# Kernel optimization log

Measured on AMD Instinct MI355X. Metric: run time of the kernel, lower is better.

Reference implementation:

```python
import jax, jax.numpy as jnp
import numpy as np

H = 1024      # hidden_size
I = 4096      # intermediate_size
E = 8         # num_experts
TOP_K = 2
LB_COEF = 0.01


def setup_inputs() -> dict:
    key = jax.random.key(0)
    ks = jax.random.split(key, 8)
    s_h = 1.0 / np.sqrt(H)
    s_i = 1.0 / np.sqrt(I)
    return {
        "x": jax.random.normal(ks[0], (2, 2048, H), dtype=jnp.float32),
        "Wr": jax.random.normal(ks[1], (H, E), dtype=jnp.float32) * s_h,
        "br": jnp.zeros((E,), dtype=jnp.float32),
        "W1": jax.random.normal(ks[2], (E, H, I), dtype=jnp.float32) * s_h,
        "b1": jnp.zeros((E, I), dtype=jnp.float32),
        "W2": jax.random.normal(ks[3], (E, I, H), dtype=jnp.float32) * s_i,
        "b2": jnp.zeros((E, H), dtype=jnp.float32),
    }


def _moe_forward(x, Wr, br, W1, b1, W2, b2):
    B, S, Hd = x.shape
    x_flat = x.reshape(-1, Hd)                      # [T, H]
    T = x_flat.shape[0]

    # ---- Router: softmax probs, top-k, renormalize ----
    logits = x_flat @ Wr + br                       # [T, E]
    probs = jax.nn.softmax(logits, axis=-1)         # [T, E]
    topk_w, topk_idx = jax.lax.top_k(probs, TOP_K)  # [T, K]
    topk_w = topk_w / jnp.sum(topk_w, axis=-1, keepdims=True)

    # ---- Load-balance aux loss (switch-style) ----
    onehot = jax.nn.one_hot(topk_idx, E, dtype=x.dtype)   # [T, K, E]
    frac_tokens = onehot.mean(axis=(0, 1))                 # [E]
    frac_probs = probs.mean(axis=0)                        # [E]
    aux_loss = E * jnp.sum(frac_tokens * frac_probs) * LB_COEF

    # combine_weights[t, e] = routing weight of expert e for token t (0 if unselected)
    combine = jnp.sum(topk_w[..., None] * onehot, axis=1)  # [T, E]

    # ---- Experts: dense per-expert FFN, weighted combine ----
    out = jnp.zeros_like(x_flat)
    for e in range(E):
        h = jax.nn.gelu(x_flat @ W1[e] + b1[e])            # [T, I]
        y = h @ W2[e] + b2[e]                              # [T, H]
        out = out + y * combine[:, e:e + 1]
    return out.reshape(B, S, Hd), aux_loss


def reference(x, Wr, br, W1, b1, W2, b2):
    return _moe_forward(x, Wr, br, W1, b1, W2, b2)
```

## Files before the change

kernel.cpp:

```cpp
#include <hip/hip_runtime.h>
#include <hip/hip_bf16.h>

#define HD 1024
#define ID 4096
#define NE 8
#define NT 4096
#define NSLOT (NT*2)

typedef __attribute__((ext_vector_type(4))) float f32x4;
typedef __attribute__((ext_vector_type(8))) short bf16x8;
typedef __attribute__((ext_vector_type(4))) unsigned int u32x4;
typedef __attribute__((ext_vector_type(2))) unsigned int u32x2;
typedef unsigned short u16;

__device__ __forceinline__ u16 f2b(float f) {
  __hip_bfloat16 h = __float2bfloat16(f);
  return __builtin_bit_cast(unsigned short, h);
}
__device__ __forceinline__ unsigned int pack2(float a, float b) {
  return (unsigned int)f2b(a) | ((unsigned int)f2b(b) << 16);
}
__device__ __forceinline__ void gload16(const void* g, void* l) {
  __builtin_amdgcn_global_load_lds(
      (const __attribute__((address_space(1))) unsigned int*)g,
      (__attribute__((address_space(3))) unsigned int*)l, 16, 0, 0);
}
__device__ __forceinline__ float gelu_tanh(float v) {
  float c = v + 0.044715f * v * v * v;
  return 0.5f * v * (1.0f + tanhf(0.7978845608028654f * c));
}

__global__ void k_convert_x(const float* __restrict__ x, u16* __restrict__ xb) {
  int i = blockIdx.x * 256 + threadIdx.x;
  const f32x4* x4 = (const f32x4*)x;
  f32x4 a = x4[2 * i], b = x4[2 * i + 1];
  u32x4 r;
  r[0] = pack2(a[0], a[1]); r[1] = pack2(a[2], a[3]);
  r[2] = pack2(b[0], b[1]); r[3] = pack2(b[2], b[3]);
  ((u32x4*)xb)[i] = r;
}

__global__ __launch_bounds__(256) void k_transpose_bf16(
    const float* __restrict__ src, u16* __restrict__ dst, int R, int C) {
  __shared__ float tile[64][65];
  int e = blockIdx.z;
  int c0 = blockIdx.x * 64;
  int r0 = blockIdx.y * 64;
  int t = threadIdx.x;
  const float* s = src + (size_t)e * R * C;
#pragma unroll
  for (int i = 0; i < 16; ++i) {
    int r = i * 4 + (t >> 6);
    tile[r][t & 63] = s[(size_t)(r0 + r) * C + c0 + (t & 63)];
  }
  __syncthreads();
  u16* d = dst + (size_t)e * R * C;
#pragma unroll
  for (int i = 0; i < 4; ++i) {
    int c = i * 16 + (t >> 4);
    int rb = (t & 15) * 4;
    u32x2 p;
    p[0] = pack2(tile[rb + 0][c], tile[rb + 1][c]);
    p[1] = pack2(tile[rb + 2][c], tile[rb + 3][c]);
    *(u32x2*)&d[(size_t)(c0 + c) * R + r0 + rb] = p;
  }
}

__global__ __launch_bounds__(256) void k_router(
    const float* __restrict__ x, const float* __restrict__ Wr,
    const float* __restrict__ br, int* __restrict__ cnt,
    int* __restrict__ slotE, int* __restrict__ slotLoc,
    float* __restrict__ slotW, float* __restrict__ probsAll) {
  __shared__ float wrt[NE * HD];
  int t = threadIdx.x;
  for (int i = t; i < NE * HD; i += 256) wrt[(i & 7) * HD + (i >> 3)] = Wr[i];
  __syncthreads();
  int wave = t >> 6, lane = t & 63;
  int token = blockIdx.x * 4 + wave;
  const float* xr = x + (size_t)token * HD;
  float acc[NE] = {0, 0, 0, 0, 0, 0, 0, 0};
#pragma unroll 4
  for (int j = 0; j < 16; ++j) {
    int h = j * 64 + lane;
    float xv = xr[h];
#pragma unroll
    for (int e = 0; e < NE; ++e) acc[e] += xv * wrt[e * HD + h];
  }
#pragma unroll
  for (int d = 1; d < 64; d <<= 1) {
#pragma unroll
    for (int e = 0; e < NE; ++e) acc[e] += __shfl_xor(acc[e], d, 64);
  }
  if (lane == 0) {
    float lg[NE], p[NE];
    float m = -1e30f;
#pragma unroll
    for (int e = 0; e < NE; ++e) { lg[e] = acc[e] + br[e]; m = fmaxf(m, lg[e]); }
    float s = 0.f;
#pragma unroll
    for (int e = 0; e < NE; ++e) { p[e] = expf(lg[e] - m); s += p[e]; }
    float inv = 1.0f / s;
    int i1 = 0, i2 = -1;
    float v1 = -1.f, v2 = -1.f;
#pragma unroll
    for (int e = 0; e < NE; ++e) {
      p[e] *= inv;
      probsAll[token * NE + e] = p[e];
      if (p[e] > v1) { v2 = v1; i2 = i1; v1 = p[e]; i1 = e; }
      else if (p[e] > v2) { v2 = p[e]; i2 = e; }
    }
    float wsum = v1 + v2;
    int l1 = atomicAdd(&cnt[i1], 1);
    int l2 = atomicAdd(&cnt[i2], 1);
    slotE[token * 2] = i1;     slotLoc[token * 2] = l1;     slotW[token * 2] = v1 / wsum;
    slotE[token * 2 + 1] = i2; slotLoc[token * 2 + 1] = l2; slotW[token * 2 + 1] = v2 / wsum;
  }
}

__global__ __launch_bounds__(256) void k_finalize(
    const float* __restrict__ probsAll, const int* __restrict__ cnt,
    int* __restrict__ off, float* __restrict__ out_aux) {
  __shared__ float red[256];
  int t = threadIdx.x;
  float loc[NE] = {0, 0, 0, 0, 0, 0, 0, 0};
  for (int i = t; i < NT; i += 256) {
#pragma unroll
    for (int e = 0; e < NE; ++e) loc[e] += probsAll[i * NE + e];
  }
  __shared__ float psum[NE];
  for (int e = 0; e < NE; ++e) {
    red[t] = loc[e];
    __syncthreads();
    for (int s = 128; s > 0; s >>= 1) {
      if (t < s) red[t] += red[t + s];
      __syncthreads();
    }
    if (t == 0) psum[e] = red[0];
    __syncthreads();
  }
  if (t == 0) {
    int o = 0;
    float a = 0.f;
    for (int e = 0; e < NE; ++e) {
      off[e] = o;
      o += cnt[e];
      a += ((float)cnt[e] / (float)NSLOT) * (psum[e] / (float)NT);
    }
    off[NE] = o;
    out_aux[0] = (float)NE * a * 0.01f;
  }
}

__global__ void k_scatter(const int* __restrict__ slotE, const int* __restrict__ slotLoc,
                          const float* __restrict__ slotW, const int* __restrict__ off,
                          int* __restrict__ rowTok, float* __restrict__ rowW) {
  int i = blockIdx.x * 256 + threadIdx.x;
  int pos = off[slotE[i]] + slotLoc[i];
  if (pos < 0) pos = 0;
  if (pos >= NSLOT) pos = NSLOT - 1;
  rowTok[pos] = i >> 1;
  rowW[pos] = slotW[i];
}

__global__ __launch_bounds__(256, 2) void k_gemm1(
    const u16* __restrict__ xb, const u16* __restrict__ w1t,
    const float* __restrict__ b1, u16* __restrict__ hbuf,
    const int* __restrict__ cnt, const int* __restrict__ off,
    const int* __restrict__ rowTok) {
  const int NWG = NE * 32 * 32;
  int bid = blockIdx.x;
  int wg = (bid & 7) * (NWG / 8) + (bid >> 3);
  int e = wg >> 10;
  int rem = wg & 1023;
  int m0 = (rem >> 5) * 128;
  int n0 = (rem & 31) * 128;
  int ce = cnt[e];
  if (m0 >= ce) return;
  int oe = off[e];
  __shared__ u16 As[2][128 * 32];
  __shared__ u16 Bs[2][128 * 32];
  __shared__ int rtok[128];
  int t = threadIdx.x;
  if (t < 128) {
    int r = m0 + t;
    if (r >= ce) r = ce - 1;
    int tok = rowTok[oe + r];
    rtok[t] = (tok < 0) ? 0 : (tok >= NT ? NT - 1 : tok);
  }
  __syncthreads();
  int c0 = t, c1 = t + 256;
  const u16* srcA0 = xb + (size_t)rtok[c0 >> 2] * HD + (c0 & 3) * 8;
  const u16* srcA1 = xb + (size_t)rtok[c1 >> 2] * HD + (c1 & 3) * 8;
  const u16* bb = w1t + (size_t)e * ID * HD + (size_t)n0 * HD;
  const u16* srcB0 = bb + (size_t)(c0 >> 2) * HD + (c0 & 3) * 8;
  const u16* srcB1 = bb + (size_t)(c1 >> 2) * HD + (c1 & 3) * 8;
  int wave = t >> 6, lane = t & 63;
  int wr = wave >> 1, wc = wave & 1;
  int aoff = (wr * 64 + (lane & 15)) * 32 + (lane >> 4) * 8;
  int boff = (wc * 64 + (lane & 15)) * 32 + (lane >> 4) * 8;
  f32x4 acc[4][4] = {};
  const int NK = HD / 32;
  gload16(srcA0, &As[0][c0 * 8]);
  gload16(srcA1, &As[0][c1 * 8]);
  gload16(srcB0, &Bs[0][c0 * 8]);
  gload16(srcB1, &Bs[0][c1 * 8]);
  srcA0 += 32; srcA1 += 32; srcB0 += 32; srcB1 += 32;
  __syncthreads();
  int cur = 0;
  for (int kt = 0;;) {
    if (kt + 1 < NK) {
      int nb = cur ^ 1;
      gload16(srcA0, &As[nb][c0 * 8]);
      gload16(srcA1, &As[nb][c1 * 8]);
      gload16(srcB0, &Bs[nb][c0 * 8]);
      gload16(srcB1, &Bs[nb][c1 * 8]);
      srcA0 += 32; srcA1 += 32; srcB0 += 32; srcB1 += 32;
    }
    const u16* ap = &As[cur][aoff];
    const u16* bp = &Bs[cur][boff];
    bf16x8 af[4], bfr[4];
#pragma unroll
    for (int m = 0; m < 4; ++m) af[m] = *(const bf16x8*)(ap + m * 16 * 32);
#pragma unroll
    for (int n = 0; n < 4; ++n) bfr[n] = *(const bf16x8*)(bp + n * 16 * 32);
#pragma unroll
    for (int m = 0; m < 4; ++m)
#pragma unroll
      for (int n = 0; n < 4; ++n)
        acc[m][n] = __builtin_amdgcn_mfma_f32_16x16x32_bf16(af[m], bfr[n], acc[m][n], 0, 0, 0);
    if (++kt == NK) break;
    __syncthreads();
    cur ^= 1;
  }
  const float* b1e = b1 + (size_t)e * ID + n0;
#pragma unroll
  for (int n = 0; n < 4; ++n) {
    int col = wc * 64 + n * 16 + (lane & 15);
    float bias = b1e[col];
#pragma unroll
    for (int m = 0; m < 4; ++m) {
      int rbase = wr * 64 + m * 16 + (lane >> 4) * 4;
#pragma unroll
      for (int r = 0; r < 4; ++r) {
        int grow = m0 + rbase + r;
        if (grow < ce) {
          float v = acc[m][n][r] + bias;
          hbuf[(size_t)(oe + grow) * ID + n0 + col] = f2b(gelu_tanh(v));
        }
      }
    }
  }
}

__global__ __launch_bounds__(256, 2) void k_gemm2(
    const u16* __restrict__ hbuf, const u16* __restrict__ w2t,
    const float* __restrict__ b2, float* __restrict__ out,
    const int* __restrict__ cnt, const int* __restrict__ off,
    const int* __restrict__ rowTok, const float* __restrict__ rowW) {
  const int NWG = NE * 32 * 2 * 8;
  int bid = blockIdx.x;
  int wg = (bid & 7) * (NWG / 8) + (bid >> 3);
  int e = wg >> 9;
  int rem = wg & 511;
  int m0 = (rem >> 4) * 128;
  int ks = (rem >> 3) & 1;
  int n0 = (rem & 7) * 128;
  int ce = cnt[e];
  if (m0 >= ce) return;
  int oe = off[e];
  int k0 = ks * (ID / 2);
  __shared__ u16 As[2][128 * 32];
  __shared__ u16 Bs[2][128 * 32];
  __shared__ int rtok[128];
  __shared__ float rw[128];
  int t = threadIdx.x;
  if (t < 128) {
    int r = m0 + t;
    int rc = (r < ce) ? r : ce - 1;
    int tok = rowTok[oe + rc];
    rtok[t] = (tok < 0) ? 0 : (tok >= NT ? NT - 1 : tok);
    rw[t] = (r < ce) ? rowW[oe + r] : 0.0f;
  }
  __syncthreads();
  int c0 = t, c1 = t + 256;
  int rA0 = m0 + (c0 >> 2); if (rA0 >= ce) rA0 = ce - 1;
  int rA1 = m0 + (c1 >> 2); if (rA1 >= ce) rA1 = ce - 1;
  const u16* srcA0 = hbuf + (size_t)(oe + rA0) * ID + k0 + (c0 & 3) * 8;
  const u16* srcA1 = hbuf + (size_t)(oe + rA1) * ID + k0 + (c1 & 3) * 8;
  const u16* bb = w2t + (size_t)e * HD * ID + (size_t)n0 * ID + k0;
  const u16* srcB0 = bb + (size_t)(c0 >> 2) * ID + (c0 & 3) * 8;
  const u16* srcB1 = bb + (size_t)(c1 >> 2) * ID + (c1 & 3) * 8;
  int wave = t >> 6, lane = t & 63;
  int wr = wave >> 1, wc = wave & 1;
  int aoff = (wr * 64 + (lane & 15)) * 32 + (lane >> 4) * 8;
  int boff = (wc * 64 + (lane & 15)) * 32 + (lane >> 4) * 8;
  f32x4 acc[4][4] = {};
  const int NK = (ID / 2) / 32;
  gload16(srcA0, &As[0][c0 * 8]);
  gload16(srcA1, &As[0][c1 * 8]);
  gload16(srcB0, &Bs[0][c0 * 8]);
  gload16(srcB1, &Bs[0][c1 * 8]);
  srcA0 += 32; srcA1 += 32; srcB0 += 32; srcB1 += 32;
  __syncthreads();
  int cur = 0;
  for (int kt = 0;;) {
    if (kt + 1 < NK) {
      int nb = cur ^ 1;
      gload16(srcA0, &As[nb][c0 * 8]);
      gload16(srcA1, &As[nb][c1 * 8]);
      gload16(srcB0, &Bs[nb][c0 * 8]);
      gload16(srcB1, &Bs[nb][c1 * 8]);
      srcA0 += 32; srcA1 += 32; srcB0 += 32; srcB1 += 32;
    }
    const u16* ap = &As[cur][aoff];
    const u16* bp = &Bs[cur][boff];
    bf16x8 af[4], bfr[4];
#pragma unroll
    for (int m = 0; m < 4; ++m) af[m] = *(const bf16x8*)(ap + m * 16 * 32);
#pragma unroll
    for (int n = 0; n < 4; ++n) bfr[n] = *(const bf16x8*)(bp + n * 16 * 32);
#pragma unroll
    for (int m = 0; m < 4; ++m)
#pragma unroll
      for (int n = 0; n < 4; ++n)
        acc[m][n] = __builtin_amdgcn_mfma_f32_16x16x32_bf16(af[m], bfr[n], acc[m][n], 0, 0, 0);
    if (++kt == NK) break;
    __syncthreads();
    cur ^= 1;
  }
  const float* b2e = b2 + (size_t)e * HD + n0;
#pragma unroll
  for (int n = 0; n < 4; ++n) {
    int col = wc * 64 + n * 16 + (lane & 15);
    float bias = (ks == 0) ? b2e[col] : 0.0f;
#pragma unroll
    for (int m = 0; m < 4; ++m) {
      int rbase = wr * 64 + m * 16 + (lane >> 4) * 4;
#pragma unroll
      for (int r = 0; r < 4; ++r) {
        int grow = m0 + rbase + r;
        if (grow < ce) {
          float v = (acc[m][n][r] + bias) * rw[rbase + r];
          atomicAdd(&out[(size_t)rtok[rbase + r] * HD + n0 + col], v);
        }
      }
    }
  }
}

extern "C" void kernel_launch(void* const* d_in, const int* in_sizes, int n_in,
                              void* d_out, int out_size, void* d_ws, size_t ws_size,
                              hipStream_t stream) {
  const float* x  = (const float*)d_in[0];
  const float* Wr = (const float*)d_in[1];
  const float* br = (const float*)d_in[2];
  const float* W1 = (const float*)d_in[3];
  const float* b1 = (const float*)d_in[4];
  const float* W2 = (const float*)d_in[5];
  const float* b2 = (const float*)d_in[6];
  float* out = (float*)d_out;

  char* ws = (char*)d_ws;
  size_t o = 0;
  auto alloc = [&](size_t bytes) {
    void* p = ws + o;
    o = (o + bytes + 255) & ~(size_t)255;
    return p;
  };
  u16* xb    = (u16*)alloc((size_t)NT * HD * 2);
  u16* w1t   = (u16*)alloc((size_t)NE * ID * HD * 2);
  u16* w2t   = (u16*)alloc((size_t)NE * ID * HD * 2);
  u16* hbuf  = (u16*)alloc((size_t)NSLOT * ID * 2);
  int* cnt     = (int*)alloc(NE * 4);
  int* off     = (int*)alloc(16 * 4);
  int* slotE   = (int*)alloc(NSLOT * 4);
  int* slotLoc = (int*)alloc(NSLOT * 4);
  float* slotW = (float*)alloc(NSLOT * 4);
  int* rowTok  = (int*)alloc(NSLOT * 4);
  float* rowW  = (float*)alloc(NSLOT * 4);
  float* probsAll = (float*)alloc((size_t)NT * NE * 4);

  if (ws_size < o) return;

  hipMemsetAsync(cnt, 0, NE * 4, stream);
  hipMemsetAsync(out, 0, (size_t)out_size * 4, stream);
  k_convert_x<<<(NT * HD / 8) / 256, 256, 0, stream>>>(x, xb);
  k_transpose_bf16<<<dim3(ID / 64, HD / 64, NE), 256, 0, stream>>>(W1, w1t, HD, ID);
  k_transpose_bf16<<<dim3(HD / 64, ID / 64, NE), 256, 0, stream>>>(W2, w2t, ID, HD);
  k_router<<<NT / 4, 256, 0, stream>>>(x, Wr, br, cnt, slotE, slotLoc, slotW, probsAll);
  k_finalize<<<1, 256, 0, stream>>>(probsAll, cnt, off, out + (size_t)NT * HD);
  k_scatter<<<NSLOT / 256, 256, 0, stream>>>(slotE, slotLoc, slotW, off, rowTok, rowW);
  k_gemm1<<<NE * 32 * 32, 256, 0, stream>>>(xb, w1t, b1, hbuf, cnt, off, rowTok);
  k_gemm2<<<NE * 32 * 2 * 8, 256, 0, stream>>>(hbuf, w2t, b2, out, cnt, off, rowTok, rowW);
}
```

Baseline: 536.4 us.

## Swizzle LDS tiles, deepen GEMM prefetch pipeline, parallelize router prob reduction

Both expert GEMMs now apply an XOR swizzle to the LDS tile layout to avoid bank conflicts on the MFMA fragment reads. The double-buffered loop is restructured to issue two stages up front, with explicit vmcnt waits and raw barriers, so global-to-LDS loads overlap the MFMA work. Launch bounds move to 3 waves per SIMD for occupancy, which tightens register pressure. The single-block prob-sum finalize is split into a 32-block reduction with atomics plus a tiny finalize kernel, which adds one memset and one launch.

```diff
diff --git a/kernel.cpp b/kernel.cpp
--- a/kernel.cpp
+++ b/kernel.cpp
@@ -117,34 +117,31 @@
   }
 }
 
-__global__ __launch_bounds__(256) void k_finalize(
-    const float* __restrict__ probsAll, const int* __restrict__ cnt,
-    int* __restrict__ off, float* __restrict__ out_aux) {
+__global__ __launch_bounds__(256) void k_psum(const float* __restrict__ probsAll,
+                                              float* __restrict__ psumG) {
   __shared__ float red[256];
   int t = threadIdx.x;
-  float loc[NE] = {0, 0, 0, 0, 0, 0, 0, 0};
-  for (int i = t; i < NT; i += 256) {
-#pragma unroll
-    for (int e = 0; e < NE; ++e) loc[e] += probsAll[i * NE + e];
-  }
-  __shared__ float psum[NE];
-  for (int e = 0; e < NE; ++e) {
-    red[t] = loc[e];
+  int base = blockIdx.x * 128;
+  float s = 0.f;
+  for (int i = t >> 3; i < 128; i += 32) s += probsAll[(base + i) * NE + (t & 7)];
+  red[t] = s;
+  __syncthreads();
+  for (int st = 128; st >= 8; st >>= 1) {
+    if (t < st) red[t] += red[t + st];
     __syncthreads();
-    for (int s = 128; s > 0; s >>= 1) {
-      if (t < s) red[t] += red[t + s];
-      __syncthreads();
-    }
-    if (t == 0) psum[e] = red[0];
-    __syncthreads();
-  }
-  if (t == 0) {
+  }
+  if (t < 8) atomicAdd(&psumG[t], red[t]);
+}
+
+__global__ void k_finalize(const float* __restrict__ psumG, const int* __restrict__ cnt,
+                           int* __restrict__ off, float* __restrict__ out_aux) {
+  if (threadIdx.x == 0) {
     int o = 0;
     float a = 0.f;
     for (int e = 0; e < NE; ++e) {
       off[e] = o;
       o += cnt[e];
-      a += ((float)cnt[e] / (float)NSLOT) * (psum[e] / (float)NT);
+      a += ((float)cnt[e] / (float)NSLOT) * (psumG[e] / (float)NT);
     }
     off[NE] = o;
     out_aux[0] = (float)NE * a * 0.01f;
@@ -162,7 +159,15 @@
   rowW[pos] = slotW[i];
 }
 
-__global__ __launch_bounds__(256, 2) void k_gemm1(
+#define STG(bf) do { \
+    gload16(srcA0, &As[bf][c0 * 8]); \
+    gload16(srcA1, &As[bf][c1 * 8]); \
+    gload16(srcB0, &Bs[bf][c0 * 8]); \
+    gload16(srcB1, &Bs[bf][c1 * 8]); \
+    srcA0 += 32; srcA1 += 32; srcB0 += 32; srcB1 += 32; \
+  } while (0)
+
+__global__ __launch_bounds__(256, 3) void k_gemm1(
     const u16* __restrict__ xb, const u16* __restrict__ w1t,
     const float* __restrict__ b1, u16* __restrict__ hbuf,
     const int* __restrict__ cnt, const int* __restrict__ off,
@@ -189,35 +194,31 @@
   }
   __syncthreads();
   int c0 = t, c1 = t + 256;
-  const u16* srcA0 = xb + (size_t)rtok[c0 >> 2] * HD + (c0 & 3) * 8;
-  const u16* srcA1 = xb + (size_t)rtok[c1 >> 2] * HD + (c1 & 3) * 8;
+  int js0 = (c0 & 3) ^ ((c0 >> 3) & 3);
+  int js1 = (c1 & 3) ^ ((c1 >> 3) & 3);
+  const u16* srcA0 = xb + (size_t)rtok[c0 >> 2] * HD + js0 * 8;
+  const u16* srcA1 = xb + (size_t)rtok[c1 >> 2] * HD + js1 * 8;
   const u16* bb = w1t + (size_t)e * ID * HD + (size_t)n0 * HD;
-  const u16* srcB0 = bb + (size_t)(c0 >> 2) * HD + (c0 & 3) * 8;
-  const u16* srcB1 = bb + (size_t)(c1 >> 2) * HD + (c1 & 3) * 8;
+  const u16* srcB0 = bb + (size_t)(c0 >> 2) * HD + js0 * 8;
+  const u16* srcB1 = bb + (size_t)(c1 >> 2) * HD + js1 * 8;
   int wave = t >> 6, lane = t & 63;
   int wr = wave >> 1, wc = wave & 1;
-  int aoff = (wr * 64 + (lane & 15)) * 32 + (lane >> 4) * 8;
-  int boff = (wc * 64 + (lane & 15)) * 32 + (lane >> 4) * 8;
+  int arow = wr * 64 + (lane & 15);
+  int aoff = arow * 32 + ((lane >> 4) ^ ((arow >> 1) & 3)) * 8;
+  int brow = wc * 64 + (lane & 15);
+  int boff = brow * 32 + ((lane >> 4) ^ ((brow >> 1) & 3)) * 8;
   f32x4 acc[4][4] = {};
   const int NK = HD / 32;
-  gload16(srcA0, &As[0][c0 * 8]);
-  gload16(srcA1, &As[0][c1 * 8]);
-  gload16(srcB0, &Bs[0][c0 * 8]);
-  gload16(srcB1, &Bs[0][c1 * 8]);
-  srcA0 += 32; srcA1 += 32; srcB0 += 32; srcB1 += 32;
-  __syncthreads();
-  int cur = 0;
-  for (int kt = 0;;) {
-    if (kt + 1 < NK) {
-      int nb = cur ^ 1;
-      gload16(srcA0, &As[nb][c0 * 8]);
-      gload16(srcA1, &As[nb][c1 * 8]);
-      gload16(srcB0, &Bs[nb][c0 * 8]);
-      gload16(srcB1, &Bs[nb][c1 * 8]);
-      srcA0 += 32; srcA1 += 32; srcB0 += 32; srcB1 += 32;
-    }
-    const u16* ap = &As[cur][aoff];
-    const u16* bp = &Bs[cur][boff];
+  STG(0);
+  STG(1);
+#pragma unroll 2
+  for (int kt = 0; kt < NK; ++kt) {
+    if (kt + 1 < NK) asm volatile("s_waitcnt vmcnt(4)" ::: "memory");
+    else             asm volatile("s_waitcnt vmcnt(0)" ::: "memory");
+    __builtin_amdgcn_s_barrier();
+    int cb = kt & 1;
+    const u16* ap = &As[cb][aoff];
+    const u16* bp = &Bs[cb][boff];
     bf16x8 af[4], bfr[4];
 #pragma unroll
     for (int m = 0; m < 4; ++m) af[m] = *(const bf16x8*)(ap + m * 16 * 32);
@@ -228,9 +229,10 @@
 #pragma unroll
       for (int n = 0; n < 4; ++n)
         acc[m][n] = __builtin_amdgcn_mfma_f32_16x16x32_bf16(af[m], bfr[n], acc[m][n], 0, 0, 0);
-    if (++kt == NK) break;
-    __syncthreads();
-    cur ^= 1;
+    if (kt + 2 < NK) {
+      __builtin_amdgcn_s_barrier();
+      STG(cb);
+    }
   }
   const float* b1e = b1 + (size_t)e * ID + n0;
 #pragma unroll
@@ -252,7 +254,7 @@
   }
 }
 
-__global__ __launch_bounds__(256, 2) void k_gemm2(
+__global__ __launch_bounds__(256, 3) void k_gemm2(
     const u16* __restrict__ hbuf, const u16* __restrict__ w2t,
     const float* __restrict__ b2, float* __restrict__ out,
     const int* __restrict__ cnt, const int* __restrict__ off,
@@ -283,37 +285,33 @@
   }
   __syncthreads();
   int c0 = t, c1 = t + 256;
+  int js0 = (c0 & 3) ^ ((c0 >> 3) & 3);
+  int js1 = (c1 & 3) ^ ((c1 >> 3) & 3);
   int rA0 = m0 + (c0 >> 2); if (rA0 >= ce) rA0 = ce - 1;
   int rA1 = m0 + (c1 >> 2); if (rA1 >= ce) rA1 = ce - 1;
-  const u16* srcA0 = hbuf + (size_t)(oe + rA0) * ID + k0 + (c0 & 3) * 8;
-  const u16* srcA1 = hbuf + (size_t)(oe + rA1) * ID + k0 + (c1 & 3) * 8;
+  const u16* srcA0 = hbuf + (size_t)(oe + rA0) * ID + k0 + js0 * 8;
+  const u16* srcA1 = hbuf + (size_t)(oe + rA1) * ID + k0 + js1 * 8;
   const u16* bb = w2t + (size_t)e * HD * ID + (size_t)n0 * ID + k0;
-  const u16* srcB0 = bb + (size_t)(c0 >> 2) * ID + (c0 & 3) * 8;
-  const u16* srcB1 = bb + (size_t)(c1 >> 2) * ID + (c1 & 3) * 8;
+  const u16* srcB0 = bb + (size_t)(c0 >> 2) * ID + js0 * 8;
+  const u16* srcB1 = bb + (size_t)(c1 >> 2) * ID + js1 * 8;
   int wave = t >> 6, lane = t & 63;
   int wr = wave >> 1, wc = wave & 1;
-  int aoff = (wr * 64 + (lane & 15)) * 32 + (lane >> 4) * 8;
-  int boff = (wc * 64 + (lane & 15)) * 32 + (lane >> 4) * 8;
+  int arow = wr * 64 + (lane & 15);
+  int aoff = arow * 32 + ((lane >> 4) ^ ((arow >> 1) & 3)) * 8;
+  int brow = wc * 64 + (lane & 15);
+  int boff = brow * 32 + ((lane >> 4) ^ ((brow >> 1) & 3)) * 8;
   f32x4 acc[4][4] = {};
   const int NK = (ID / 2) / 32;
-  gload16(srcA0, &As[0][c0 * 8]);
-  gload16(srcA1, &As[0][c1 * 8]);
-  gload16(srcB0, &Bs[0][c0 * 8]);
-  gload16(srcB1, &Bs[0][c1 * 8]);
-  srcA0 += 32; srcA1 += 32; srcB0 += 32; srcB1 += 32;
-  __syncthreads();
-  int cur = 0;
-  for (int kt = 0;;) {
-    if (kt + 1 < NK) {
-      int nb = cur ^ 1;
-      gload16(srcA0, &As[nb][c0 * 8]);
-      gload16(srcA1, &As[nb][c1 * 8]);
-      gload16(srcB0, &Bs[nb][c0 * 8]);
-      gload16(srcB1, &Bs[nb][c1 * 8]);
-      srcA0 += 32; srcA1 += 32; srcB0 += 32; srcB1 += 32;
-    }
-    const u16* ap = &As[cur][aoff];
-    const u16* bp = &Bs[cur][boff];
+  STG(0);
+  STG(1);
+#pragma unroll 2
+  for (int kt = 0; kt < NK; ++kt) {
+    if (kt + 1 < NK) asm volatile("s_waitcnt vmcnt(4)" ::: "memory");
+    else             asm volatile("s_waitcnt vmcnt(0)" ::: "memory");
+    __builtin_amdgcn_s_barrier();
+    int cb = kt & 1;
+    const u16* ap = &As[cb][aoff];
+    const u16* bp = &Bs[cb][boff];
     bf16x8 af[4], bfr[4];
 #pragma unroll
     for (int m = 0; m < 4; ++m) af[m] = *(const bf16x8*)(ap + m * 16 * 32);
@@ -324,9 +322,10 @@
 #pragma unroll
       for (int n = 0; n < 4; ++n)
         acc[m][n] = __builtin_amdgcn_mfma_f32_16x16x32_bf16(af[m], bfr[n], acc[m][n], 0, 0, 0);
-    if (++kt == NK) break;
-    __syncthreads();
-    cur ^= 1;
+    if (kt + 2 < NK) {
+      __builtin_amdgcn_s_barrier();
+      STG(cb);
+    }
   }
   const float* b2e = b2 + (size_t)e * HD + n0;
 #pragma unroll
@@ -372,6 +371,7 @@
   u16* w2t   = (u16*)alloc((size_t)NE * ID * HD * 2);
   u16* hbuf  = (u16*)alloc((size_t)NSLOT * ID * 2);
   int* cnt     = (int*)alloc(NE * 4);
+  float* psumG = (float*)alloc(NE * 4);
   int* off     = (int*)alloc(16 * 4);
   int* slotE   = (int*)alloc(NSLOT * 4);
   int* slotLoc = (int*)alloc(NSLOT * 4);
@@ -383,12 +383,14 @@
   if (ws_size < o) return;
 
   hipMemsetAsync(cnt, 0, NE * 4, stream);
+  hipMemsetAsync(psumG, 0, NE * 4, stream);
   hipMemsetAsync(out, 0, (size_t)out_size * 4, stream);
   k_convert_x<<<(NT * HD / 8) / 256, 256, 0, stream>>>(x, xb);
   k_transpose_bf16<<<dim3(ID / 64, HD / 64, NE), 256, 0, stream>>>(W1, w1t, HD, ID);
   k_transpose_bf16<<<dim3(HD / 64, ID / 64, NE), 256, 0, stream>>>(W2, w2t, ID, HD);
   k_router<<<NT / 4, 256, 0, stream>>>(x, Wr, br, cnt, slotE, slotLoc, slotW, probsAll);
-  k_finalize<<<1, 256, 0, stream>>>(probsAll, cnt, off, out + (size_t)NT * HD);
+  k_psum<<<32, 256, 0, stream>>>(probsAll, psumG);
+  k_finalize<<<1, 64, 0, stream>>>(psumG, cnt, off, out + (size_t)NT * HD);
   k_scatter<<<NSLOT / 256, 256, 0, stream>>>(slotE, slotLoc, slotW, off, rowTok, rowW);
   k_gemm1<<<NE * 32 * 32, 256, 0, stream>>>(xb, w1t, b1, hbuf, cnt, off, rowTok);
   k_gemm2<<<NE * 32 * 2 * 8, 256, 0, stream>>>(hbuf, w2t, b2, out, cnt, off, rowTok, rowW);
```

Measured after the change: 518.6 us. -3.3%, faster.
